# Optimization experiments

Hardware: AMD Instinct MI355X
Metric: run time of the kernel (lower is better)

## Reference

```python
import jax, jax.numpy as jnp
import numpy as np

N_NODES = 100000
N_EDGES = 1600000
D_FEAT = 256
UNITS = 128


def setup_inputs() -> dict:
    key = jax.random.key(0)
    k1, k2, k3, k4, k5 = jax.random.split(key, 5)
    x = jax.random.normal(k1, (N_NODES, D_FEAT), dtype=jnp.float32)
    # glorot-scale init for w (scale doesn't affect correctness checking)
    w = jax.random.normal(k2, (D_FEAT, UNITS), dtype=jnp.float32) * (2.0 / (D_FEAT + UNITS)) ** 0.5
    adj_src = jax.random.randint(k3, (N_EDGES,), 0, N_NODES, dtype=jnp.int64)
    adj_dst = jax.random.randint(k4, (N_EDGES,), 0, N_NODES, dtype=jnp.int64)
    adj_vals = jax.random.uniform(k5, (N_EDGES,), dtype=jnp.float32)
    return {"x": x, "w": w, "adj_src": adj_src, "adj_dst": adj_dst, "adj_vals": adj_vals}


def reference(x, w, adj_src, adj_dst, adj_vals):
    # x: [N, D], w: [D, U]  -> dense projection
    h = x @ w  # [N, U]
    # sparse_dense_matmul(adj_norm, h): out[i] = sum_j A[i,j] * h[j]
    # COO: edge e contributes adj_vals[e] * h[adj_src[e]] to row adj_dst[e]
    msgs = adj_vals[:, None] * h[adj_src]  # [E, U]
    out = jax.ops.segment_sum(msgs, adj_dst, num_segments=N_NODES)  # [N, U]
    return out
```

## Files before the change

### kernel.cpp

```cpp
#include <hip/hip_runtime.h>

#define D_FEAT 256
#define UNITS  128

#define NBITS  7
#define BINSZ  128
#define BINCAP 2432
#define MAXNB  800

typedef __attribute__((ext_vector_type(8))) short short8;
typedef __attribute__((ext_vector_type(4))) float floatx4;

__device__ inline ushort f2bf(float f) {
    uint u = __float_as_uint(f);
    uint r = u + 0x7FFF + ((u >> 16) & 1);
    return (ushort)(r >> 16);
}

__global__ __launch_bounds__(256) void wt_prep_kernel(const float* __restrict__ w,
                                                      ushort* __restrict__ wT,
                                                      int* __restrict__ cursor, int ncur) {
    int idx = blockIdx.x * 256 + threadIdx.x;
    int n = idx >> 8;
    int k = idx & 255;
    wT[n * 256 + k] = f2bf(w[(size_t)k * UNITS + n]);
    if (idx < ncur) cursor[idx] = 0;
}

__global__ __launch_bounds__(512, 4) void gemm_mfma4_kernel(const float* __restrict__ x,
                                                            const ushort* __restrict__ wT,
                                                            ushort* __restrict__ hb, int M) {
    __shared__ ushort lds_w[128 * 256];

    const int tid  = threadIdx.x;
    const int wave = tid >> 6;
    const int lane = tid & 63;
    const int quad = lane >> 4;
    const int m16  = lane & 15;

    const int row  = blockIdx.x * 128 + wave * 16 + m16;
    const int rowc = row < M ? row : M - 1;
    const float* xr = x + (size_t)rowc * D_FEAT;

    short8 wv[8];
    #pragma unroll
    for (int r = 0; r < 8; ++r)
        wv[r] = *(const short8*)(wT + (size_t)(r * 512 + tid) * 8);
    __builtin_amdgcn_sched_barrier(0);

    float4 xv[16];
    #pragma unroll
    for (int s = 0; s < 8; ++s) {
        const float4* p = (const float4*)(xr + s * 32 + quad * 8);
        xv[2 * s]     = p[0];
        xv[2 * s + 1] = p[1];
    }
    __builtin_amdgcn_sched_barrier(0);

    #pragma unroll
    for (int r = 0; r < 8; ++r) {
        int ci = r * 512 + tid;
        int n  = ci >> 5;
        int ts = (ci & 31) ^ (n & 7);
        *(short8*)(lds_w + n * 256 + ts * 8) = wv[r];
    }
    __builtin_amdgcn_sched_barrier(0);

    short8 afrag[8];
    #pragma unroll
    for (int s = 0; s < 8; ++s) {
        float4 lo = xv[2 * s];
        float4 hi = xv[2 * s + 1];
        union { short8 v; ushort u[8]; } af;
        af.u[0] = f2bf(lo.x); af.u[1] = f2bf(lo.y);
        af.u[2] = f2bf(lo.z); af.u[3] = f2bf(lo.w);
        af.u[4] = f2bf(hi.x); af.u[5] = f2bf(hi.y);
        af.u[6] = f2bf(hi.z); af.u[7] = f2bf(hi.w);
        afrag[s] = af.v;
    }

    __syncthreads();

    floatx4 acc[8] = {};
    #pragma unroll
    for (int s = 0; s < 8; ++s) {
        #pragma unroll
        for (int c = 0; c < 8; ++c) {
            int rowb = c * 16 + m16;
            int ts   = (s * 4 + quad) ^ (m16 & 7);
            short8 bfrag = *(const short8*)(lds_w + rowb * 256 + ts * 8);
            acc[c] = __builtin_amdgcn_mfma_f32_16x16x32_bf16(afrag[s], bfrag, acc[c], 0, 0, 0);
        }
    }

    #pragma unroll
    for (int c = 0; c < 8; ++c) {
        #pragma unroll
        for (int i = 0; i < 4; ++i) {
            int r = blockIdx.x * 128 + wave * 16 + quad * 4 + i;
            if (r < M) hb[(size_t)r * UNITS + c * 16 + m16] = f2bf(acc[c][i]);
        }
    }
}

__global__ __launch_bounds__(1024) void coarse_scatter_kernel(const int* __restrict__ src,
                                                              const int* __restrict__ dst,
                                                              const float* __restrict__ vals,
                                                              int* __restrict__ cursor,
                                                              int2* __restrict__ staged,
                                                              int E, int NB, int chunk) {
    __shared__ int s_hist[MAXNB];
    __shared__ int s_base[MAXNB];

    const int tid = threadIdx.x;
    const int T   = 1024;
    const int e0 = blockIdx.x * chunk;
    const int e1 = min(E, e0 + chunk);

    for (int i = tid; i < NB; i += T) s_hist[i] = 0;
    __syncthreads();

    for (int e = e0 + tid; e < e1; e += T)
        atomicAdd(&s_hist[dst[e] >> NBITS], 1);
    __syncthreads();

    for (int b = tid; b < NB; b += T) {
        int c = s_hist[b];
        s_base[b] = (c > 0) ? atomicAdd(&cursor[b * 4], c) : 0;
    }
    __syncthreads();
    for (int i = tid; i < NB; i += T) s_hist[i] = 0;
    __syncthreads();

    for (int e = e0 + tid; e < e1; e += T) {
        int d = dst[e];
        int b = d >> NBITS;
        int r = s_base[b] + atomicAdd(&s_hist[b], 1);
        if (r < BINCAP) {
            int meta = src[e] | ((d & (BINSZ - 1)) << 20);
            staged[(size_t)b * BINCAP + r] = make_int2(meta, __float_as_int(vals[e]));
        }
    }
}

#define ACC8(h, v)                                  \
    a0 += (v) * __uint_as_float((h).x << 16);       \
    a1 += (v) * __uint_as_float((h).x & 0xFFFF0000u); \
    a2 += (v) * __uint_as_float((h).y << 16);       \
    a3 += (v) * __uint_as_float((h).y & 0xFFFF0000u); \
    a4 += (v) * __uint_as_float((h).z << 16);       \
    a5 += (v) * __uint_as_float((h).z & 0xFFFF0000u); \
    a6 += (v) * __uint_as_float((h).w << 16);       \
    a7 += (v) * __uint_as_float((h).w & 0xFFFF0000u);

__global__ __launch_bounds__(512) void gather_sort_kernel(const int* __restrict__ cursor,
                                                          const int2* __restrict__ staged,
                                                          const ushort* __restrict__ hb,
                                                          float* __restrict__ out, int N) {
    __shared__ int2 sraw[BINCAP];
    __shared__ int2 sbuf[BINCAP];
    __shared__ int cnt[BINSZ], ofs[BINSZ], cur[BINSZ];
    __shared__ int gofs[16];

    const int b   = blockIdx.x;
    const int tid = threadIdx.x;

    int n = cursor[b * 4];
    if (n > BINCAP) n = BINCAP;

    for (int i = tid; i < BINSZ; i += 512) cnt[i] = 0;
    __syncthreads();

    const int2* sg = staged + (size_t)b * BINCAP;

    for (int i = tid; i < n; i += 512) {
        int2 e = sg[i];
        sraw[i] = e;
        atomicAdd(&cnt[(e.x >> 20) & (BINSZ - 1)], 1);
    }
    __syncthreads();

    if (tid < 16) {
        int s = 0;
        #pragma unroll
        for (int j = 0; j < 8; ++j) s += cnt[tid * 8 + j];
        gofs[tid] = s;
    }
    __syncthreads();
    if (tid == 0) {
        int run = 0;
        #pragma unroll
        for (int g = 0; g < 16; ++g) { int c = gofs[g]; gofs[g] = run; run += c; }
    }
    __syncthreads();
    if (tid < 16) {
        int run = gofs[tid];
        #pragma unroll
        for (int j = 0; j < 8; ++j) {
            int d = tid * 8 + j;
            int c = cnt[d];
            ofs[d] = run; cur[d] = run; run += c;
        }
    }
    __syncthreads();

    for (int i = tid; i < n; i += 512) {
        int2 e = sraw[i];
        int pos = atomicAdd(&cur[(e.x >> 20) & (BINSZ - 1)], 1);
        sbuf[pos] = e;
    }
    __syncthreads();

    const int ex = (tid >> 6) * 4 + ((tid & 63) >> 4);
    const int m  = tid & 15;

    #pragma unroll
    for (int r = 0; r < 4; ++r) {
        int d  = r * 32 + ex;
        int dg = b * BINSZ + d;
        if (dg >= N) continue;
        int start = ofs[d];
        int c     = cnt[d];

        float a0 = 0.f, a1 = 0.f, a2 = 0.f, a3 = 0.f;
        float a4 = 0.f, a5 = 0.f, a6 = 0.f, a7 = 0.f;
        int j = 0;
        for (; j + 8 <= c; j += 8) {
            int2 e0 = sbuf[start + j];
            int2 e1 = sbuf[start + j + 1];
            int2 e2 = sbuf[start + j + 2];
            int2 e3 = sbuf[start + j + 3];
            int2 e4 = sbuf[start + j + 4];
            int2 e5 = sbuf[start + j + 5];
            int2 e6 = sbuf[start + j + 6];
            int2 e7 = sbuf[start + j + 7];
            __builtin_amdgcn_sched_barrier(0);
            uint4 h0 = *(const uint4*)(hb + (size_t)(e0.x & 0xFFFFF) * UNITS + m * 8);
            uint4 h1 = *(const uint4*)(hb + (size_t)(e1.x & 0xFFFFF) * UNITS + m * 8);
            uint4 h2 = *(const uint4*)(hb + (size_t)(e2.x & 0xFFFFF) * UNITS + m * 8);
            uint4 h3 = *(const uint4*)(hb + (size_t)(e3.x & 0xFFFFF) * UNITS + m * 8);
            uint4 h4 = *(const uint4*)(hb + (size_t)(e4.x & 0xFFFFF) * UNITS + m * 8);
            uint4 h5 = *(const uint4*)(hb + (size_t)(e5.x & 0xFFFFF) * UNITS + m * 8);
            uint4 h6 = *(const uint4*)(hb + (size_t)(e6.x & 0xFFFFF) * UNITS + m * 8);
            uint4 h7 = *(const uint4*)(hb + (size_t)(e7.x & 0xFFFFF) * UNITS + m * 8);
            __builtin_amdgcn_sched_barrier(0);
            float v0 = __int_as_float(e0.y);
            float v1 = __int_as_float(e1.y);
            float v2 = __int_as_float(e2.y);
            float v3 = __int_as_float(e3.y);
            float v4 = __int_as_float(e4.y);
            float v5 = __int_as_float(e5.y);
            float v6 = __int_as_float(e6.y);
            float v7 = __int_as_float(e7.y);
            ACC8(h0, v0)
            ACC8(h1, v1)
            ACC8(h2, v2)
            ACC8(h3, v3)
            ACC8(h4, v4)
            ACC8(h5, v5)
            ACC8(h6, v6)
            ACC8(h7, v7)
        }
        if (j + 4 <= c) {
            int2 e0 = sbuf[start + j];
            int2 e1 = sbuf[start + j + 1];
            int2 e2 = sbuf[start + j + 2];
            int2 e3 = sbuf[start + j + 3];
            __builtin_amdgcn_sched_barrier(0);
            uint4 h0 = *(const uint4*)(hb + (size_t)(e0.x & 0xFFFFF) * UNITS + m * 8);
            uint4 h1 = *(const uint4*)(hb + (size_t)(e1.x & 0xFFFFF) * UNITS + m * 8);
            uint4 h2 = *(const uint4*)(hb + (size_t)(e2.x & 0xFFFFF) * UNITS + m * 8);
            uint4 h3 = *(const uint4*)(hb + (size_t)(e3.x & 0xFFFFF) * UNITS + m * 8);
            __builtin_amdgcn_sched_barrier(0);
            float v0 = __int_as_float(e0.y);
            float v1 = __int_as_float(e1.y);
            float v2 = __int_as_float(e2.y);
            float v3 = __int_as_float(e3.y);
            ACC8(h0, v0)
            ACC8(h1, v1)
            ACC8(h2, v2)
            ACC8(h3, v3)
            j += 4;
        }
        for (; j < c; ++j) {
            int2 e0 = sbuf[start + j];
            uint4 h0 = *(const uint4*)(hb + (size_t)(e0.x & 0xFFFFF) * UNITS + m * 8);
            float v0 = __int_as_float(e0.y);
            ACC8(h0, v0)
        }

        float* op = out + (size_t)dg * UNITS + m * 8;
        *(floatx4*)op       = (floatx4){a0, a1, a2, a3};
        *(floatx4*)(op + 4) = (floatx4){a4, a5, a6, a7};
    }
}

extern "C" void kernel_launch(void* const* d_in, const int* in_sizes, int n_in,
                              void* d_out, int out_size, void* d_ws, size_t ws_size,
                              hipStream_t stream) {
    const float* x        = (const float*)d_in[0];
    const float* w        = (const float*)d_in[1];
    const int*   adj_src  = (const int*)d_in[2];
    const int*   adj_dst  = (const int*)d_in[3];
    const float* adj_vals = (const float*)d_in[4];
    float*       out      = (float*)d_out;

    const int M = in_sizes[0] / D_FEAT;
    const int E = in_sizes[2];
    const int NB = (M + BINSZ - 1) >> NBITS;

    char*   ws  = (char*)d_ws;
    ushort* hb  = (ushort*)ws;
    size_t  off = (size_t)M * UNITS * sizeof(ushort);
    off = (off + 255) & ~(size_t)255;
    ushort* wT  = (ushort*)(ws + off);
    off += (size_t)128 * 256 * sizeof(ushort);
    int*    cursor = (int*)(ws + off);
    off += (size_t)NB * 4 * sizeof(int);
    off = (off + 15) & ~(size_t)15;
    int2*   staged = (int2*)(ws + off);

    wt_prep_kernel<<<128, 256, 0, stream>>>(w, wT, cursor, NB * 4);

    gemm_mfma4_kernel<<<(M + 127) / 128, 512, 0, stream>>>(x, wT, hb, M);

    const int NSCAT = 256;
    const int chunk = (E + NSCAT - 1) / NSCAT;
    coarse_scatter_kernel<<<NSCAT, 1024, 0, stream>>>(adj_src, adj_dst, adj_vals,
                                                      cursor, staged, E, NB, chunk);

    gather_sort_kernel<<<NB, 512, 0, stream>>>(cursor, staged, hb, out, M);
}
```

Before: 283.9 us.

## Fuse GEMM and coarse edge scatter into one heterogeneous kernel launch

```diff
diff --git a/kernel.cpp b/kernel.cpp
--- a/kernel.cpp
+++ b/kernel.cpp
@@ -27,18 +27,63 @@
     if (idx < ncur) cursor[idx] = 0;
 }
 
-__global__ __launch_bounds__(512, 4) void gemm_mfma4_kernel(const float* __restrict__ x,
-                                                            const ushort* __restrict__ wT,
-                                                            ushort* __restrict__ hb, int M) {
-    __shared__ ushort lds_w[128 * 256];
-
-    const int tid  = threadIdx.x;
+__global__ __launch_bounds__(512, 4) void gemm_scatter2_kernel(
+        const float* __restrict__ x, const ushort* __restrict__ wT,
+        ushort* __restrict__ hb, int M,
+        const int* __restrict__ src, const int* __restrict__ dst,
+        const float* __restrict__ vals,
+        int* __restrict__ cursor, int2* __restrict__ staged,
+        int E, int NB, int chunk) {
+    __shared__ __align__(16) char smem[65536];
+    const int tid = threadIdx.x;
+    const int bid = blockIdx.x;
+
+    const bool is_scatter = (bid < 512) && (bid & 1);
+
+    if (is_scatter) {
+        int* s_hist = (int*)smem;
+        int* s_base = s_hist + MAXNB;
+        const int T  = 512;
+        const int sb = bid >> 1;
+        const int e0 = sb * chunk;
+        const int e1 = min(E, e0 + chunk);
+
+        for (int i = tid; i < NB; i += T) s_hist[i] = 0;
+        __syncthreads();
+
+        for (int e = e0 + tid; e < e1; e += T)
+            atomicAdd(&s_hist[dst[e] >> NBITS], 1);
+        __syncthreads();
+
+        for (int b = tid; b < NB; b += T) {
+            int c = s_hist[b];
+            s_base[b] = (c > 0) ? atomicAdd(&cursor[b * 4], c) : 0;
+        }
+        __syncthreads();
+        for (int i = tid; i < NB; i += T) s_hist[i] = 0;
+        __syncthreads();
+
+        for (int e = e0 + tid; e < e1; e += T) {
+            int d = dst[e];
+            int b = d >> NBITS;
+            int r = s_base[b] + atomicAdd(&s_hist[b], 1);
+            if (r < BINCAP) {
+                int meta = src[e] | ((d & (BINSZ - 1)) << 20);
+                staged[(size_t)b * BINCAP + r] = make_int2(meta, __float_as_int(vals[e]));
+            }
+        }
+        return;
+    }
+
+    ushort* lds_w = (ushort*)smem;
+
+    const int gb   = (bid < 512) ? (bid >> 1) : (bid - 256);
     const int wave = tid >> 6;
     const int lane = tid & 63;
     const int quad = lane >> 4;
     const int m16  = lane & 15;
 
-    const int row  = blockIdx.x * 128 + wave * 16 + m16;
+    const int row  = gb * 128 + wave * 16 + m16;
     const int rowc = row < M ? row : M - 1;
     const float* xr = x + (size_t)rowc * D_FEAT;
 
@@ -97,48 +142,8 @@
     for (int c = 0; c < 8; ++c) {
         #pragma unroll
         for (int i = 0; i < 4; ++i) {
-            int r = blockIdx.x * 128 + wave * 16 + quad * 4 + i;
+            int r = gb * 128 + wave * 16 + quad * 4 + i;
             if (r < M) hb[(size_t)r * UNITS + c * 16 + m16] = f2bf(acc[c][i]);
-        }
-    }
-}
-
-__global__ __launch_bounds__(1024) void coarse_scatter_kernel(const int* __restrict__ src,
-                                                              const int* __restrict__ dst,
-                                                              const float* __restrict__ vals,
-                                                              int* __restrict__ cursor,
-                                                              int2* __restrict__ staged,
-                                                              int E, int NB, int chunk) {
-    __shared__ int s_hist[MAXNB];
-    __shared__ int s_base[MAXNB];
-
-    const int tid = threadIdx.x;
-    const int T   = 1024;
-    const int e0 = blockIdx.x * chunk;
-    const int e1 = min(E, e0 + chunk);
-
-    for (int i = tid; i < NB; i += T) s_hist[i] = 0;
-    __syncthreads();
-
-    for (int e = e0 + tid; e < e1; e += T)
-        atomicAdd(&s_hist[dst[e] >> NBITS], 1);
-    __syncthreads();
-
-    for (int b = tid; b < NB; b += T) {
-        int c = s_hist[b];
-        s_base[b] = (c > 0) ? atomicAdd(&cursor[b * 4], c) : 0;
-    }
-    __syncthreads();
-    for (int i = tid; i < NB; i += T) s_hist[i] = 0;
-    __syncthreads();
-
-    for (int e = e0 + tid; e < e1; e += T) {
-        int d = dst[e];
-        int b = d >> NBITS;
-        int r = s_base[b] + atomicAdd(&s_hist[b], 1);
-        if (r < BINCAP) {
-            int meta = src[e] | ((d & (BINSZ - 1)) << 20);
-            staged[(size_t)b * BINCAP + r] = make_int2(meta, __float_as_int(vals[e]));
         }
     }
 }
@@ -322,12 +327,11 @@
 
     wt_prep_kernel<<<128, 256, 0, stream>>>(w, wT, cursor, NB * 4);
 
-    gemm_mfma4_kernel<<<(M + 127) / 128, 512, 0, stream>>>(x, wT, hb, M);
-
     const int NSCAT = 256;
     const int chunk = (E + NSCAT - 1) / NSCAT;
-    coarse_scatter_kernel<<<NSCAT, 1024, 0, stream>>>(adj_src, adj_dst, adj_vals,
-                                                      cursor, staged, E, NB, chunk);
+    const int NGEMM = (M + 127) / 128;
+    gemm_scatter2_kernel<<<NSCAT + NGEMM, 512, 0, stream>>>(
+        x, wT, hb, M, adj_src, adj_dst, adj_vals, cursor, staged, E, NB, chunk);
 
     gather_sort_kernel<<<NB, 512, 0, stream>>>(cursor, staged, hb, out, M);
 }
```

Measured after the change: 289.9 us. +2.1%, slower.
